# Kernel tuning notes

Measured on AMD Instinct MI355X. Metric: run time of the kernel, lower is better.

The kernel has to match this reference:

```python
import jax, jax.numpy as jnp
import numpy as np

B = 4096
NUM_FEATURES = 2048
NUM_NEURONS = 1024
NUM_TARGETS = 8
NNZ1 = 65536
NNZ2 = 8192


def _sparse_linear(x, w, b, rows, cols, n_out):
    """y[b, o] = sum_{e: rows[e]==o} w[e] * x[b, cols[e]] + b[o].

    x: [B, n_in], w: [nnz], rows/cols: [nnz] int, b: [n_out].
    """
    prod = x[:, cols] * w  # [B, nnz] gather + elementwise
    # segment_sum reduces over leading axis -> work on [nnz, B]
    y = jax.ops.segment_sum(prod.T, rows, num_segments=n_out)  # [n_out, B]
    return y.T + b


def setup_inputs() -> dict:
    key = jax.random.key(0)
    ks = jax.random.split(key, 9)
    x = jax.random.normal(ks[0], (B, NUM_FEATURES), dtype=jnp.float32)
    w1 = jax.random.normal(ks[1], (NNZ1,), dtype=jnp.float32) * 0.05
    b1 = jax.random.normal(ks[2], (NUM_NEURONS,), dtype=jnp.float32) * 0.05
    w2 = jax.random.normal(ks[3], (NNZ2,), dtype=jnp.float32) * 0.05
    b2 = jax.random.normal(ks[4], (NUM_TARGETS,), dtype=jnp.float32) * 0.05
    conn1_out = jax.random.randint(ks[5], (NNZ1,), 0, NUM_NEURONS, dtype=jnp.int64 if jax.config.jax_enable_x64 else jnp.int32)
    conn1_in = jax.random.randint(ks[6], (NNZ1,), 0, NUM_FEATURES, dtype=conn1_out.dtype)
    conn2_out = jax.random.randint(ks[7], (NNZ2,), 0, NUM_TARGETS, dtype=conn1_out.dtype)
    conn2_in = jax.random.randint(ks[8], (NNZ2,), 0, NUM_NEURONS, dtype=conn1_out.dtype)
    return {
        "x": x, "w1": w1, "b1": b1, "w2": w2, "b2": b2,
        "conn1_out": conn1_out, "conn1_in": conn1_in,
        "conn2_out": conn2_out, "conn2_in": conn2_in,
    }


def reference(x, w1, b1, w2, b2, conn1_out, conn1_in, conn2_out, conn2_in):
    h = jax.nn.sigmoid(_sparse_linear(x, w1, b1, conn1_out, conn1_in, b1.shape[0]))
    out = _sparse_linear(h, w2, b2, conn2_out, conn2_in, b2.shape[0])
    # num_targets = 8 != 1, so no final sigmoid (matches CrossEntropyLoss path)
    return out
```

## Files before the change

### kernel.cpp

```cpp
#include <hip/hip_runtime.h>
#include <math.h>

#define BATCH 4096
#define NFEAT 2048
#define NNEUR 1024
#define NTGT  8
#define NNZ1  65536
#define NNZ2  8192

#define BM 128
#define BN 64
#define BK 64
#define KSTEPS (NFEAT / BK)

typedef short  bf16x8 __attribute__((ext_vector_type(8)));
typedef float  f32x4  __attribute__((ext_vector_type(4)));

#define OFF_W1F  ((size_t)0)
#define OFF_W2D  ((size_t)8388608)
#define OFF_W1B  ((size_t)8421376)
#define OFF_PART ((size_t)29392896)

#define ZERO_FLOAT4 526336

__device__ __forceinline__ unsigned short f2bf(float f) {
    union { float f; unsigned int u; } a; a.f = f;
    unsigned int u = a.u;
    u += 0x7fffu + ((u >> 16) & 1u);
    return (unsigned short)(u >> 16);
}

__device__ __forceinline__ uint4 pk8(float4 lo, float4 hi) {
    uint4 r;
    asm("v_cvt_pk_bf16_f32 %0, %1, %2" : "=v"(r.x) : "v"(lo.x), "v"(lo.y));
    asm("v_cvt_pk_bf16_f32 %0, %1, %2" : "=v"(r.y) : "v"(lo.z), "v"(lo.w));
    asm("v_cvt_pk_bf16_f32 %0, %1, %2" : "=v"(r.z) : "v"(hi.x), "v"(hi.y));
    asm("v_cvt_pk_bf16_f32 %0, %1, %2" : "=v"(r.w) : "v"(hi.z), "v"(hi.w));
    return r;
}

__global__ void k_zero4(float4* __restrict__ p) {
    int i = blockIdx.x * blockDim.x + threadIdx.x;
    p[i] = make_float4(0.f, 0.f, 0.f, 0.f);
}

__global__ void k_build(const float* __restrict__ w1, const int* __restrict__ c1o,
                        const int* __restrict__ c1i,
                        const float* __restrict__ w2, const int* __restrict__ c2o,
                        const int* __restrict__ c2i,
                        float* __restrict__ W1f, float* __restrict__ W2d) {
    int i = blockIdx.x * blockDim.x + threadIdx.x;
    if (i < NNZ1) {
        atomicAdd(&W1f[(size_t)c1o[i] * NFEAT + c1i[i]], w1[i]);
    } else {
        int j = i - NNZ1;
        if (j < NNZ2) atomicAdd(&W2d[c2i[j] * NTGT + c2o[j]], w2[j]);
    }
}

__global__ void k_convert(const float* __restrict__ W1f, unsigned short* __restrict__ W1b) {
    int i = blockIdx.x * blockDim.x + threadIdx.x;
    float4 v = ((const float4*)W1f)[i];
    ushort4 o;
    o.x = f2bf(v.x); o.y = f2bf(v.y); o.z = f2bf(v.z); o.w = f2bf(v.w);
    ((ushort4*)W1b)[i] = o;
}

__global__ __launch_bounds__(256) void k_gemm(const unsigned short* __restrict__ W1b,
                                              const float* __restrict__ x,
                                              const float* __restrict__ b1,
                                              const float* __restrict__ W2d,
                                              float* __restrict__ partial) {
    __shared__ unsigned short ldsA[2][BM * BK];
    __shared__ unsigned short ldsB[2][BN * BK];
    __shared__ float s_w2[BM][NTGT];
    __shared__ float s_b1[BM];
    __shared__ float s_pt[2][BN][NTGT];

    int bid = blockIdx.x;
    int v   = bid >> 3;
    int n0  = ((bid & 7) * 8 + (v >> 3)) * BN;
    int mt  = v & 7;
    int m0  = mt * BM;

    int tid  = threadIdx.x;
    int wv   = tid >> 6;
    int lane = tid & 63;
    int wm = wv >> 1, wn = wv & 1;
    int lr = lane & 15, lg = lane >> 4;

    for (int i = tid; i < BM * NTGT; i += 256)
        s_w2[i >> 3][i & 7] = W2d[(m0 + (i >> 3)) * NTGT + (i & 7)];
    if (tid < BM) s_b1[tid] = b1[m0 + tid];
    asm volatile("s_waitcnt vmcnt(0) lgkmcnt(0)" ::: "memory");
    __builtin_amdgcn_sched_barrier(0);

    f32x4 zero4 = {0.f, 0.f, 0.f, 0.f};
    f32x4 acc[4][2];
#pragma unroll
    for (int i = 0; i < 4; ++i)
#pragma unroll
        for (int j = 0; j < 2; ++j) acc[i][j] = zero4;

    int r0 = tid >> 3, s0 = tid & 7;
    const unsigned short* gA0 = &W1b[(size_t)(m0 + r0) * NFEAT + s0 * 8];
    const unsigned short* gA1 = gA0 + 32 * NFEAT;
    const unsigned short* gA2 = gA0 + 64 * NFEAT;
    const unsigned short* gA3 = gA0 + 96 * NFEAT;
    const float* gB0 = &x[(size_t)(n0 + r0) * NFEAT + s0 * 8];
    const float* gB1 = gB0 + 32 * NFEAT;
    const int iw0 = r0 * 8 + (s0 ^ (r0 & 7));
    const int iw1 = iw0 + 256, iw2 = iw0 + 512, iw3 = iw0 + 768;

    bf16x8 A0a, A0b, A0c, A0d;  float4 B0a, B0b, B0c, B0d;
    bf16x8 A1a, A1b, A1c, A1d;  float4 B1a, B1b, B1c, B1d;
    bf16x8 af0[4], af1[4], bg0[2], bg1[2];

#define LOADS0(T) do { int kk = (T) * BK;                           \
        A0a = *(const bf16x8*)(gA0 + kk); A0b = *(const bf16x8*)(gA1 + kk); \
        A0c = *(const bf16x8*)(gA2 + kk); A0d = *(const bf16x8*)(gA3 + kk); \
        B0a = *(const float4*)(gB0 + kk); B0b = *(const float4*)(gB0 + kk + 4); \
        B0c = *(const float4*)(gB1 + kk); B0d = *(const float4*)(gB1 + kk + 4); } while (0)
#define LOADS1(T) do { int kk = (T) * BK;                           \
        A1a = *(const bf16x8*)(gA0 + kk); A1b = *(const bf16x8*)(gA1 + kk); \
        A1c = *(const bf16x8*)(gA2 + kk); A1d = *(const bf16x8*)(gA3 + kk); \
        B1a = *(const float4*)(gB0 + kk); B1b = *(const float4*)(gB0 + kk + 4); \
        B1c = *(const float4*)(gB1 + kk); B1d = *(const float4*)(gB1 + kk + 4); } while (0)

#define STORE0(BUF) do {                                            \
        bf16x8* dA = (bf16x8*)&ldsA[BUF][0];                        \
        dA[iw0] = A0a; dA[iw1] = A0b; dA[iw2] = A0c; dA[iw3] = A0d; \
        uint4* dB = (uint4*)&ldsB[BUF][0];                          \
        dB[iw0] = pk8(B0a, B0b); dB[iw1] = pk8(B0c, B0d); } while (0)
#define STORE1(BUF) do {                                            \
        bf16x8* dA = (bf16x8*)&ldsA[BUF][0];                        \
        dA[iw0] = A1a; dA[iw1] = A1b; dA[iw2] = A1c; dA[iw3] = A1d; \
        uint4* dB = (uint4*)&ldsB[BUF][0];                          \
        dB[iw0] = pk8(B1a, B1b); dB[iw1] = pk8(B1c, B1d); } while (0)

#define READF(BUF) do {                                             \
        const unsigned short* bA = ldsA[BUF];                       \
        const unsigned short* bB = ldsB[BUF];                       \
        _Pragma("unroll")                                           \
        for (int i = 0; i < 4; ++i) {                               \
            int rowa = wm * 64 + i * 16 + lr;                       \
            af0[i] = *(const bf16x8*)&bA[(rowa * 8 + ((lg)     ^ (rowa & 7))) * 8]; \
            af1[i] = *(const bf16x8*)&bA[(rowa * 8 + ((4 + lg) ^ (rowa & 7))) * 8]; \
        }                                                           \
        _Pragma("unroll")                                           \
        for (int j = 0; j < 2; ++j) {                               \
            int rowb = wn * 32 + j * 16 + lr;                       \
            bg0[j] = *(const bf16x8*)&bB[(rowb * 8 + ((lg)     ^ (rowb & 7))) * 8]; \
            bg1[j] = *(const bf16x8*)&bB[(rowb * 8 + ((4 + lg) ^ (rowb & 7))) * 8]; \
        }                                                           \
    } while (0)

#define MFMAS() do {                                                \
        _Pragma("unroll")                                           \
        for (int i = 0; i < 4; ++i)                                 \
            _Pragma("unroll")                                       \
            for (int j = 0; j < 2; ++j)                             \
                acc[i][j] = __builtin_amdgcn_mfma_f32_16x16x32_bf16(af0[i], bg0[j], acc[i][j], 0, 0, 0); \
        _Pragma("unroll")                                           \
        for (int i = 0; i < 4; ++i)                                 \
            _Pragma("unroll")                                       \
            for (int j = 0; j < 2; ++j)                             \
                acc[i][j] = __builtin_amdgcn_mfma_f32_16x16x32_bf16(af1[i], bg1[j], acc[i][j], 0, 0, 0); \
    } while (0)

#define WAIT_VM(N)  asm volatile("s_waitcnt vmcnt(" #N ")" ::: "memory"); \
                    __builtin_amdgcn_sched_barrier(0)
#define WAIT_LGKM() asm volatile("s_waitcnt lgkmcnt(0)" ::: "memory");    \
                    __builtin_amdgcn_sched_barrier(0)

    LOADS0(0);
    LOADS1(1);
    WAIT_VM(8);
    STORE0(0);
    WAIT_LGKM();
    __builtin_amdgcn_s_barrier();

#pragma unroll 1
    for (int t = 0; t < KSTEPS - 2; t += 2) {
        LOADS0(t + 2);
        __builtin_amdgcn_sched_barrier(0);
        READF(0);
        WAIT_LGKM();
        __builtin_amdgcn_s_setprio(1); MFMAS(); __builtin_amdgcn_s_setprio(0);
        __builtin_amdgcn_sched_barrier(0);
        WAIT_VM(8);
        STORE1(1);
        WAIT_LGKM();
        __builtin_amdgcn_s_barrier();
        LOADS1(t + 3);
        __builtin_amdgcn_sched_barrier(0);
        READF(1);
        WAIT_LGKM();
        __builtin_amdgcn_s_setprio(1); MFMAS(); __builtin_amdgcn_s_setprio(0);
        __builtin_amdgcn_sched_barrier(0);
        WAIT_VM(8);
        STORE0(0);
        WAIT_LGKM();
        __builtin_amdgcn_s_barrier();
    }
    READF(0);
    WAIT_LGKM();
    __builtin_amdgcn_s_setprio(1); MFMAS(); __builtin_amdgcn_s_setprio(0);
    __builtin_amdgcn_sched_barrier(0);
    WAIT_VM(0);
    STORE1(1);
    WAIT_LGKM();
    __builtin_amdgcn_s_barrier();
    READF(1);
    WAIT_LGKM();
    __builtin_amdgcn_s_setprio(1); MFMAS(); __builtin_amdgcn_s_setprio(0);
    __builtin_amdgcn_sched_barrier(0);

#undef LOADS0
#undef LOADS1
#undef STORE0
#undef STORE1
#undef READF
#undef MFMAS
#undef WAIT_VM
#undef WAIT_LGKM

    float pt[2][NTGT];
#pragma unroll
    for (int j = 0; j < 2; ++j)
#pragma unroll
        for (int t = 0; t < NTGT; ++t) pt[j][t] = 0.f;

#pragma unroll
    for (int i = 0; i < 4; ++i) {
#pragma unroll
        for (int r = 0; r < 4; ++r) {
            int ml = wm * 64 + i * 16 + lg * 4 + r;
            float bn = s_b1[ml];
#pragma unroll
            for (int j = 0; j < 2; ++j) {
                float h = 1.f / (1.f + __expf(-(acc[i][j][r] + bn)));
#pragma unroll
                for (int t = 0; t < NTGT; ++t)
                    pt[j][t] += h * s_w2[ml][t];
            }
        }
    }
#pragma unroll
    for (int j = 0; j < 2; ++j)
#pragma unroll
        for (int t = 0; t < NTGT; ++t) {
            float val = pt[j][t];
            val += __shfl_xor(val, 16, 64);
            val += __shfl_xor(val, 32, 64);
            pt[j][t] = val;
        }
    if (lg == 0) {
#pragma unroll
        for (int j = 0; j < 2; ++j) {
            int nl = wn * 32 + j * 16 + lr;
#pragma unroll
            for (int t = 0; t < NTGT; ++t)
                s_pt[wm][nl][t] = pt[j][t];
        }
    }
    __syncthreads();
    for (int idx = tid; idx < BN * NTGT; idx += 256) {
        int nl = idx >> 3, t = idx & 7;
        partial[((size_t)mt * BATCH + (n0 + nl)) * NTGT + t] = s_pt[0][nl][t] + s_pt[1][nl][t];
    }
}

__global__ void k_reduce(const float* __restrict__ partial, const float* __restrict__ b2,
                         float* __restrict__ out) {
    int i = blockIdx.x * blockDim.x + threadIdx.x;
    float v = b2[i & 7];
#pragma unroll
    for (int c = 0; c < 8; ++c) v += partial[(size_t)c * BATCH * NTGT + i];
    out[i] = v;
}

extern "C" void kernel_launch(void* const* d_in, const int* in_sizes, int n_in,
                              void* d_out, int out_size, void* d_ws, size_t ws_size,
                              hipStream_t stream) {
    (void)in_sizes; (void)n_in; (void)out_size; (void)ws_size;
    const float* x   = (const float*)d_in[0];
    const float* w1  = (const float*)d_in[1];
    const float* b1  = (const float*)d_in[2];
    const float* w2  = (const float*)d_in[3];
    const float* b2  = (const float*)d_in[4];
    const int*   c1o = (const int*)d_in[5];
    const int*   c1i = (const int*)d_in[6];
    const int*   c2o = (const int*)d_in[7];
    const int*   c2i = (const int*)d_in[8];
    float* out = (float*)d_out;

    char* ws = (char*)d_ws;
    float*          W1f  = (float*)(ws + OFF_W1F);
    float*          W2d  = (float*)(ws + OFF_W2D);
    unsigned short* W1b  = (unsigned short*)(ws + OFF_W1B);
    float*          part = (float*)(ws + OFF_PART);

    k_zero4<<<ZERO_FLOAT4 / 256, 256, 0, stream>>>((float4*)ws);

    k_build<<<(NNZ1 + NNZ2) / 256, 256, 0, stream>>>(w1, c1o, c1i, w2, c2o, c2i, W1f, W2d);

    k_convert<<<NNEUR * NFEAT / 4 / 256, 256, 0, stream>>>(W1f, W1b);

    k_gemm<<<(NNEUR / BM) * (BATCH / BN), 256, 0, stream>>>(W1b, x, b1, W2d, part);

    k_reduce<<<BATCH * NTGT / 256, 256, 0, stream>>>(part, b2, out);
}
```

Baseline: 53.33 us.

## Fold final reduction into GEMM via atomics and restructure pipeline waits

Removes the separate reduce kernel and partial buffer: the output is initialized with b2 in the zero kernel and each GEMM block atomically adds its per-M-tile contribution. The main loop is reordered so the LDS store of the next stage comes before the fragment reads and MFMAs, with explicit vmcnt waits, sched_barriers and setprio removed, leaving only lgkmcnt fences. This saves one launch and a round trip through global memory. The cost is atomic contention (8 adders per output) and scheduling left to the compiler, which may insert conservative waits.

Result: faster. 50.41 us (median of 2 runs) (-5.5%).

```diff
diff --git a/kernel.cpp b/kernel.cpp
--- a/kernel.cpp
+++ b/kernel.cpp
@@ -19,9 +19,9 @@
 #define OFF_W1F  ((size_t)0)
 #define OFF_W2D  ((size_t)8388608)
 #define OFF_W1B  ((size_t)8421376)
-#define OFF_PART ((size_t)29392896)
 
 #define ZERO_FLOAT4 526336
+#define OUT_FLOAT4  (BATCH * NTGT / 4)
 
 __device__ __forceinline__ unsigned short f2bf(float f) {
     union { float f; unsigned int u; } a; a.f = f;
@@ -39,9 +39,18 @@
     return r;
 }
 
-__global__ void k_zero4(float4* __restrict__ p) {
+__global__ void k_zero(float4* __restrict__ ws4, float4* __restrict__ out4,
+                       const float* __restrict__ b2) {
     int i = blockIdx.x * blockDim.x + threadIdx.x;
-    p[i] = make_float4(0.f, 0.f, 0.f, 0.f);
+    if (i < ZERO_FLOAT4) {
+        ws4[i] = make_float4(0.f, 0.f, 0.f, 0.f);
+    } else {
+        int j = i - ZERO_FLOAT4;
+        if (j < OUT_FLOAT4) {
+            int p = (j & 1) * 4;
+            out4[j] = make_float4(b2[p], b2[p + 1], b2[p + 2], b2[p + 3]);
+        }
+    }
 }
 
 __global__ void k_build(const float* __restrict__ w1, const int* __restrict__ c1o,
@@ -70,7 +79,7 @@
                                               const float* __restrict__ x,
                                               const float* __restrict__ b1,
                                               const float* __restrict__ W2d,
-                                              float* __restrict__ partial) {
+                                              float* __restrict__ out) {
     __shared__ unsigned short ldsA[2][BM * BK];
     __shared__ unsigned short ldsB[2][BN * BK];
     __shared__ float s_w2[BM][NTGT];
@@ -92,8 +101,6 @@
     for (int i = tid; i < BM * NTGT; i += 256)
         s_w2[i >> 3][i & 7] = W2d[(m0 + (i >> 3)) * NTGT + (i & 7)];
     if (tid < BM) s_b1[tid] = b1[m0 + tid];
-    asm volatile("s_waitcnt vmcnt(0) lgkmcnt(0)" ::: "memory");
-    __builtin_amdgcn_sched_barrier(0);
 
     f32x4 zero4 = {0.f, 0.f, 0.f, 0.f};
     f32x4 acc[4][2];
@@ -168,53 +175,37 @@
                 acc[i][j] = __builtin_amdgcn_mfma_f32_16x16x32_bf16(af1[i], bg1[j], acc[i][j], 0, 0, 0); \
     } while (0)
 
-#define WAIT_VM(N)  asm volatile("s_waitcnt vmcnt(" #N ")" ::: "memory"); \
-                    __builtin_amdgcn_sched_barrier(0)
-#define WAIT_LGKM() asm volatile("s_waitcnt lgkmcnt(0)" ::: "memory");    \
-                    __builtin_amdgcn_sched_barrier(0)
+#define LDSFENCE() asm volatile("s_waitcnt lgkmcnt(0)" ::: "memory")
 
     LOADS0(0);
     LOADS1(1);
-    WAIT_VM(8);
     STORE0(0);
-    WAIT_LGKM();
+    LDSFENCE();
     __builtin_amdgcn_s_barrier();
 
 #pragma unroll 1
-    for (int t = 0; t < KSTEPS - 2; t += 2) {
-        LOADS0(t + 2);
-        __builtin_amdgcn_sched_barrier(0);
+    for (int p = 0; p < 15; ++p) {
+        int e = 2 * p;
+        LOADS0(e + 2);
+        STORE1(1);
         READF(0);
-        WAIT_LGKM();
-        __builtin_amdgcn_s_setprio(1); MFMAS(); __builtin_amdgcn_s_setprio(0);
-        __builtin_amdgcn_sched_barrier(0);
-        WAIT_VM(8);
-        STORE1(1);
-        WAIT_LGKM();
+        MFMAS();
+        LDSFENCE();
         __builtin_amdgcn_s_barrier();
-        LOADS1(t + 3);
-        __builtin_amdgcn_sched_barrier(0);
+        LOADS1(e + 3);
+        STORE0(0);
         READF(1);
-        WAIT_LGKM();
-        __builtin_amdgcn_s_setprio(1); MFMAS(); __builtin_amdgcn_s_setprio(0);
-        __builtin_amdgcn_sched_barrier(0);
-        WAIT_VM(8);
-        STORE0(0);
-        WAIT_LGKM();
+        MFMAS();
+        LDSFENCE();
         __builtin_amdgcn_s_barrier();
     }
+    STORE1(1);
     READF(0);
-    WAIT_LGKM();
-    __builtin_amdgcn_s_setprio(1); MFMAS(); __builtin_amdgcn_s_setprio(0);
-    __builtin_amdgcn_sched_barrier(0);
-    WAIT_VM(0);
-    STORE1(1);
-    WAIT_LGKM();
+    MFMAS();
+    LDSFENCE();
     __builtin_amdgcn_s_barrier();
     READF(1);
-    WAIT_LGKM();
-    __builtin_amdgcn_s_setprio(1); MFMAS(); __builtin_amdgcn_s_setprio(0);
-    __builtin_amdgcn_sched_barrier(0);
+    MFMAS();
 
 #undef LOADS0
 #undef LOADS1
@@ -222,8 +213,7 @@
 #undef STORE1
 #undef READF
 #undef MFMAS
-#undef WAIT_VM
-#undef WAIT_LGKM
+#undef LDSFENCE
 
     float pt[2][NTGT];
 #pragma unroll
@@ -267,17 +257,8 @@
     __syncthreads();
     for (int idx = tid; idx < BN * NTGT; idx += 256) {
         int nl = idx >> 3, t = idx & 7;
-        partial[((size_t)mt * BATCH + (n0 + nl)) * NTGT + t] = s_pt[0][nl][t] + s_pt[1][nl][t];
-    }
-}
-
-__global__ void k_reduce(const float* __restrict__ partial, const float* __restrict__ b2,
-                         float* __restrict__ out) {
-    int i = blockIdx.x * blockDim.x + threadIdx.x;
-    float v = b2[i & 7];
-#pragma unroll
-    for (int c = 0; c < 8; ++c) v += partial[(size_t)c * BATCH * NTGT + i];
-    out[i] = v;
+        atomicAdd(&out[(size_t)(n0 + nl) * NTGT + t], s_pt[0][nl][t] + s_pt[1][nl][t]);
+    }
 }
 
 extern "C" void kernel_launch(void* const* d_in, const int* in_sizes, int n_in,
@@ -299,15 +280,13 @@
     float*          W1f  = (float*)(ws + OFF_W1F);
     float*          W2d  = (float*)(ws + OFF_W2D);
     unsigned short* W1b  = (unsigned short*)(ws + OFF_W1B);
-    float*          part = (float*)(ws + OFF_PART);
-
-    k_zero4<<<ZERO_FLOAT4 / 256, 256, 0, stream>>>((float4*)ws);
+
+    k_zero<<<(ZERO_FLOAT4 + OUT_FLOAT4 + 255) / 256, 256, 0, stream>>>(
+        (float4*)ws, (float4*)out, b2);
 
     k_build<<<(NNZ1 + NNZ2) / 256, 256, 0, stream>>>(w1, c1o, c1i, w2, c2o, c2i, W1f, W2d);
 
     k_convert<<<NNEUR * NFEAT / 4 / 256, 256, 0, stream>>>(W1f, W1b);
 
-    k_gemm<<<(NNEUR / BM) * (BATCH / BN), 256, 0, stream>>>(W1b, x, b1, W2d, part);
-
-    k_reduce<<<BATCH * NTGT / 256, 256, 0, stream>>>(part, b2, out);
-}
+    k_gemm<<<(NNEUR / BM) * (BATCH / BN), 256, 0, stream>>>(W1b, x, b1, W2d, out);
+}
```
